# Kernel tuning notes

Measured on AMD Instinct MI355X. Metric: run time of the kernel, lower is better.

## Reference

```python
import jax, jax.numpy as jnp
import numpy as np

B, H, T, D = 8, 16, 16, 128
S = 4096


def setup_inputs() -> dict:
    key = jax.random.key(0)
    k1, k2 = jax.random.split(key)
    # distinct, in-range positions per batch row
    input_pos = jnp.arange(B * T, dtype=jnp.int64 if jax.config.jax_enable_x64 else jnp.int32).reshape(B, T)
    k = jax.random.normal(k1, (B, H, T, D), dtype=jnp.float32)
    v = jax.random.normal(k2, (B, H, T, D), dtype=jnp.float32)
    k_cache = jnp.zeros((B, H, S, D), dtype=jnp.float32)
    v_cache = jnp.zeros((B, H, S, D), dtype=jnp.float32)
    return {"input_pos": input_pos, "k": k, "v": v, "k_cache": k_cache, "v_cache": v_cache}


def reference(input_pos, k, v, k_cache, v_cache):
    # Batched index_copy_ along dim -2 (sequence) of the (B, H, S, D) caches.
    # Advanced-index scatter: batch idx (B,1) broadcasts with input_pos (B,T)
    # -> gathered/scattered block has shape (B, T, H, D), so transpose k/v.
    n = k.shape[0]
    b_idx = jnp.arange(n)[:, None]  # (B, 1)
    k_out = k_cache.at[b_idx, :, input_pos, :].set(jnp.swapaxes(k, 1, 2))
    v_out = v_cache.at[b_idx, :, input_pos, :].set(jnp.swapaxes(v, 1, 2))
    return k_out, v_out
```

## Files before the change

kernel.cpp:

```cpp
#include <hip/hip_runtime.h>

constexpr int B = 8;
constexpr int H = 16;
constexpr int T = 16;
constexpr int D = 128;
constexpr int S = 4096;
constexpr int D4 = D / 4;
constexpr size_t CACHE_ELEMS = (size_t)B * H * S * D;
constexpr size_t CACHE_F4    = CACHE_ELEMS / 4;
constexpr int NEW_F4 = B * H * T * D4;

constexpr int TPB = 256;
constexpr int COPY_BLOCKS = 2048;
constexpr int BLOCKS_PER_HALF = COPY_BLOCKS / 2;
constexpr int UNROLL = 8;
constexpr int ITERS = 8;

__global__ void __launch_bounds__(TPB)
kv_copy_kernel(const float4* __restrict__ k_cache,
               const float4* __restrict__ v_cache,
               float4* __restrict__ out) {
    int blk = blockIdx.x;
    const float4* __restrict__ src;
    float4* __restrict__ dst;
    if (blk < BLOCKS_PER_HALF) {
        src = k_cache;
        dst = out;
    } else {
        src = v_cache;
        dst = out + CACHE_F4;
        blk -= BLOCKS_PER_HALF;
    }
    size_t base = (size_t)blk * (TPB * UNROLL * ITERS) + threadIdx.x;
    for (int it = 0; it < ITERS; ++it) {
        size_t a = base + (size_t)it * (TPB * UNROLL);
        float4 r[UNROLL];
#pragma unroll
        for (int u = 0; u < UNROLL; ++u) r[u] = src[a + (size_t)u * TPB];
#pragma unroll
        for (int u = 0; u < UNROLL; ++u) dst[a + (size_t)u * TPB] = r[u];
    }
}

__global__ void kv_scatter_kernel(const int* __restrict__ input_pos,
                                  const float4* __restrict__ k_new,
                                  const float4* __restrict__ v_new,
                                  float4* __restrict__ out_k,
                                  float4* __restrict__ out_v) {
    int i = blockIdx.x * blockDim.x + threadIdx.x;
    if (i >= NEW_F4) return;
    int d  = i % D4;
    int t  = (i / D4) % T;
    int h  = (i / (D4 * T)) % H;
    int b  = i / (D4 * T * H);
    int p  = input_pos[b * T + t];
    size_t dst = (((size_t)b * H + h) * S + p) * D4 + d;
    out_k[dst] = k_new[i];
    out_v[dst] = v_new[i];
}

extern "C" void kernel_launch(void* const* d_in, const int* in_sizes, int n_in,
                              void* d_out, int out_size, void* d_ws, size_t ws_size,
                              hipStream_t stream) {
    const int*    input_pos = (const int*)d_in[0];
    const float4* k_new     = (const float4*)d_in[1];
    const float4* v_new     = (const float4*)d_in[2];
    const float4* k_cache   = (const float4*)d_in[3];
    const float4* v_cache   = (const float4*)d_in[4];

    float* out = (float*)d_out;
    float4* out_k = (float4*)out;
    float4* out_v = (float4*)(out + CACHE_ELEMS);

    kv_copy_kernel<<<COPY_BLOCKS, TPB, 0, stream>>>(k_cache, v_cache, out_k);

    kv_scatter_kernel<<<(NEW_F4 + 255) / 256, 256, 0, stream>>>(
        input_pos, k_new, v_new, out_k, out_v);
}
```

Before: 206.8 us.

## Fuse cache copy and scatter into one kernel with nontemporal loads/stores

Merges the bulk cache copy and the positional scatter into a single kernel. Each block copies its slice of rows, synchronizes, then writes any new k/v rows whose position falls within that slice. This removes the second launch and the gap between kernels. Copy loads and stores now use nontemporal builtins so the streaming traffic bypasses the cache. The scatter relies on each block owning its copied range, so ordering within the block is enough for correctness.

```diff
diff --git a/kernel.cpp b/kernel.cpp
--- a/kernel.cpp
+++ b/kernel.cpp
@@ -8,72 +8,75 @@
 constexpr int D4 = D / 4;
 constexpr size_t CACHE_ELEMS = (size_t)B * H * S * D;
 constexpr size_t CACHE_F4    = CACHE_ELEMS / 4;
-constexpr int NEW_F4 = B * H * T * D4;
+
+typedef float f4 __attribute__((ext_vector_type(4)));
 
 constexpr int TPB = 256;
 constexpr int COPY_BLOCKS = 2048;
 constexpr int BLOCKS_PER_HALF = COPY_BLOCKS / 2;
 constexpr int UNROLL = 8;
 constexpr int ITERS = 8;
+constexpr int F4_PER_BLOCK = TPB * UNROLL * ITERS;
+constexpr int ROWS_PER_BLOCK = F4_PER_BLOCK / D4;
 
 __global__ void __launch_bounds__(TPB)
-kv_copy_kernel(const float4* __restrict__ k_cache,
-               const float4* __restrict__ v_cache,
-               float4* __restrict__ out) {
+kv_fused_kernel(const f4* __restrict__ k_cache,
+                const f4* __restrict__ v_cache,
+                const f4* __restrict__ k_new,
+                const f4* __restrict__ v_new,
+                const int* __restrict__ input_pos,
+                f4* __restrict__ out) {
     int blk = blockIdx.x;
-    const float4* __restrict__ src;
-    float4* __restrict__ dst;
+    const f4* __restrict__ src;
+    const f4* __restrict__ newsrc;
+    f4* __restrict__ dst;
     if (blk < BLOCKS_PER_HALF) {
-        src = k_cache;
-        dst = out;
+        src = k_cache; newsrc = k_new; dst = out;
     } else {
-        src = v_cache;
-        dst = out + CACHE_F4;
         blk -= BLOCKS_PER_HALF;
+        src = v_cache; newsrc = v_new; dst = out + CACHE_F4;
     }
-    size_t base = (size_t)blk * (TPB * UNROLL * ITERS) + threadIdx.x;
+
+    size_t base = (size_t)blk * F4_PER_BLOCK + threadIdx.x;
     for (int it = 0; it < ITERS; ++it) {
         size_t a = base + (size_t)it * (TPB * UNROLL);
-        float4 r[UNROLL];
+        f4 r[UNROLL];
 #pragma unroll
-        for (int u = 0; u < UNROLL; ++u) r[u] = src[a + (size_t)u * TPB];
+        for (int u = 0; u < UNROLL; ++u)
+            r[u] = __builtin_nontemporal_load(&src[a + (size_t)u * TPB]);
 #pragma unroll
-        for (int u = 0; u < UNROLL; ++u) dst[a + (size_t)u * TPB] = r[u];
+        for (int u = 0; u < UNROLL; ++u)
+            __builtin_nontemporal_store(r[u], &dst[a + (size_t)u * TPB]);
     }
-}
 
-__global__ void kv_scatter_kernel(const int* __restrict__ input_pos,
-                                  const float4* __restrict__ k_new,
-                                  const float4* __restrict__ v_new,
-                                  float4* __restrict__ out_k,
-                                  float4* __restrict__ out_v) {
-    int i = blockIdx.x * blockDim.x + threadIdx.x;
-    if (i >= NEW_F4) return;
-    int d  = i % D4;
-    int t  = (i / D4) % T;
-    int h  = (i / (D4 * T)) % H;
-    int b  = i / (D4 * T * H);
-    int p  = input_pos[b * T + t];
-    size_t dst = (((size_t)b * H + h) * S + p) * D4 + d;
-    out_k[dst] = k_new[i];
-    out_v[dst] = v_new[i];
+    __syncthreads();
+    int bh = blk >> 3;
+    int b  = bh >> 4;
+    int s0 = (blk & 7) * ROWS_PER_BLOCK;
+    int d4 = threadIdx.x & (D4 - 1);
+    int tl = threadIdx.x >> 5;
+#pragma unroll
+    for (int tg = 0; tg < T / 8; ++tg) {
+        int t = tg * 8 + tl;
+        int p = input_pos[b * T + t];
+        if (p >= s0 && p < s0 + ROWS_PER_BLOCK) {
+            dst[((size_t)bh * S + p) * D4 + d4] =
+                newsrc[((size_t)bh * T + t) * D4 + d4];
+        }
+    }
 }
 
 extern "C" void kernel_launch(void* const* d_in, const int* in_sizes, int n_in,
                               void* d_out, int out_size, void* d_ws, size_t ws_size,
                               hipStream_t stream) {
-    const int*    input_pos = (const int*)d_in[0];
-    const float4* k_new     = (const float4*)d_in[1];
-    const float4* v_new     = (const float4*)d_in[2];
-    const float4* k_cache   = (const float4*)d_in[3];
-    const float4* v_cache   = (const float4*)d_in[4];
+    const int* input_pos = (const int*)d_in[0];
+    const f4*  k_new     = (const f4*)d_in[1];
+    const f4*  v_new     = (const f4*)d_in[2];
+    const f4*  k_cache   = (const f4*)d_in[3];
+    const f4*  v_cache   = (const f4*)d_in[4];
 
-    float* out = (float*)d_out;
-    float4* out_k = (float4*)out;
-    float4* out_v = (float4*)(out + CACHE_ELEMS);
+    f4* out = (f4*)d_out;
 
-    kv_copy_kernel<<<COPY_BLOCKS, TPB, 0, stream>>>(k_cache, v_cache, out_k);
-
-    kv_scatter_kernel<<<(NEW_F4 + 255) / 256, 256, 0, stream>>>(
-        input_pos, k_new, v_new, out_k, out_v);
+    kv_fused_kernel<<<COPY_BLOCKS, TPB, 0, stream>>>(
+        k_cache, v_cache, k_new, v_new, input_pos, out);
 }
```

After: 188.6 us. 1.1x faster.
